# Kernel optimization log

Hardware: AMD Instinct MI355X
Metric: run time of the kernel (lower is better)

Reference implementation:

```python
import jax, jax.numpy as jnp
import numpy as np

N, L, D = 4096, 16, 768        # nodes, max name tokens, gpt2 embed dim
NH_NAME = 4                    # name-encoder attention heads
H, NH, NL, C = 1024, 8, 4, 16  # hidden, encoder heads, encoder layers, classes
XF = 256                       # raw node feature dim; feat_dim = XF + D = 1024
VOCAB = 50257


def _ln(x, g, b, eps=1e-5):
    m = jnp.mean(x, axis=-1, keepdims=True)
    v = jnp.var(x, axis=-1, keepdims=True)
    return (x - m) * jax.lax.rsqrt(v + eps) * g + b


def _mha(x, in_w, in_b, out_w, out_b, nh, key_mask=None):
    # x: [B, S, E]; in_w: [3E, E] (torch nn.MultiheadAttention packed qkv)
    B, S, E = x.shape
    dh = E // nh
    qkv = x @ in_w.T + in_b
    q, k, v = jnp.split(qkv, 3, axis=-1)
    q = q.reshape(B, S, nh, dh)
    k = k.reshape(B, S, nh, dh)
    v = v.reshape(B, S, nh, dh)
    scores = jnp.einsum('bqhd,bkhd->bhqk', q, k) / jnp.sqrt(jnp.asarray(dh, x.dtype))
    if key_mask is not None:
        scores = jnp.where(key_mask[:, None, None, :], scores, jnp.asarray(-1e9, x.dtype))
    a = jax.nn.softmax(scores, axis=-1)
    o = jnp.einsum('bhqk,bkhd->bqhd', a, v).reshape(B, S, E)
    return o @ out_w.T + out_b


def setup_inputs() -> dict:
    key = jax.random.key(0)
    ks = jax.random.split(key, 16)
    s = 0.02
    r = lambda i, shape: jax.random.normal(ks[i], shape, jnp.float32) * s
    return {
        'name_tokens': jax.random.randint(ks[0], (N, L), 0, VOCAB),
        'name_lens': jax.random.randint(ks[1], (N,), 1, L + 1),
        'x_feats': jax.random.normal(ks[2], (N, XF), jnp.float32),
        'wte': r(3, (VOCAB, D)),
        'mha_in_w': r(4, (3 * D, D)), 'mha_in_b': jnp.zeros((3 * D,), jnp.float32),
        'mha_out_w': r(5, (D, D)), 'mha_out_b': jnp.zeros((D,), jnp.float32),
        'bott_w': r(6, (H, XF + D)), 'bott_b': jnp.zeros((H,), jnp.float32),
        'enc_in_w': r(7, (NL, 3 * H, H)), 'enc_in_b': jnp.zeros((NL, 3 * H), jnp.float32),
        'enc_out_w': r(8, (NL, H, H)), 'enc_out_b': jnp.zeros((NL, H), jnp.float32),
        'enc_ln1_g': jnp.ones((NL, H), jnp.float32), 'enc_ln1_b': jnp.zeros((NL, H), jnp.float32),
        'enc_ln2_g': jnp.ones((NL, H), jnp.float32), 'enc_ln2_b': jnp.zeros((NL, H), jnp.float32),
        'enc_ff1_w': r(9, (NL, 2 * H, H)), 'enc_ff1_b': jnp.zeros((NL, 2 * H), jnp.float32),
        'enc_ff2_w': r(10, (NL, H, 2 * H)), 'enc_ff2_b': jnp.zeros((NL, H), jnp.float32),
        'cls_w': r(11, (C, H)), 'cls_b': jnp.zeros((C,), jnp.float32),
    }


def reference(name_tokens, name_lens, x_feats, wte,
              mha_in_w, mha_in_b, mha_out_w, mha_out_b,
              bott_w, bott_b,
              enc_in_w, enc_in_b, enc_out_w, enc_out_b,
              enc_ln1_g, enc_ln1_b, enc_ln2_g, enc_ln2_b,
              enc_ff1_w, enc_ff1_b, enc_ff2_w, enc_ff2_b,
              cls_w, cls_b):
    # --- GraphNameEncoder: batched over all N ragged name sequences ---
    mask = jnp.arange(L)[None, :] < name_lens[:, None]          # [N, L] valid-token mask
    emb = wte[name_tokens]                                      # [N, L, D]
    attn = _mha(emb, mha_in_w, mha_in_b, mha_out_w, mha_out_b, NH_NAME, key_mask=mask)
    name_emb = jnp.sum(jnp.where(mask[:, :, None], attn, 0.0), axis=1)  # [N, D]
    x = jnp.concatenate([x_feats, name_emb], axis=-1)           # [N, XF + D]
    # --- bottleneck ---
    x = x @ bott_w.T + bott_b                                   # [N, H]
    # --- TransformerEncoder on seq_len=1 (x.unsqueeze(1)), post-norm, relu ---
    h = x[:, None, :]                                           # [N, 1, H]
    for l in range(NL):
        a = _mha(h, enc_in_w[l], enc_in_b[l], enc_out_w[l], enc_out_b[l], NH)
        h = _ln(h + a, enc_ln1_g[l], enc_ln1_b[l])
        f = jax.nn.relu(h @ enc_ff1_w[l].T + enc_ff1_b[l]) @ enc_ff2_w[l].T + enc_ff2_b[l]
        h = _ln(h + f, enc_ln2_g[l], enc_ln2_b[l])
    out = h @ cls_w.T + cls_b                                   # [N, 1, C]
    return out[:, 0, :]                                         # squeeze -> [N, C]
```

## Files before the change

kernel.cpp:

```cpp
#include <hip/hip_runtime.h>

typedef unsigned short bf16_t;
typedef __attribute__((ext_vector_type(8))) __bf16 bf16x8;
typedef __attribute__((ext_vector_type(4))) float f32x4;

__device__ __forceinline__ float bf2f(unsigned v) { return __uint_as_float(v << 16); }
__device__ __forceinline__ bf16_t f2bf(float f) {
  unsigned u = __float_as_uint(f);
  return (bf16_t)((u + 0x7fffu + ((u >> 16) & 1u)) >> 16);
}
__device__ __forceinline__ unsigned pack2(float a, float b) {
  return (unsigned)f2bf(a) | ((unsigned)f2bf(b) << 16);
}

__device__ __forceinline__ void swz_decode(int& mt, int& nt) {
  const int NT = gridDim.x, MT = gridDim.y;
  int lin = blockIdx.y * NT + blockIdx.x;
  if ((MT & 7) == 0 && gridDim.z == 1) {
    int xcd = lin & 7;
    int j = lin >> 3;
    mt = (j / NT) * 8 + xcd;
    nt = j % NT;
  } else {
    mt = blockIdx.y;
    nt = blockIdx.x;
  }
}

__global__ __launch_bounds__(256) void scan_lens(const int* __restrict__ lens,
                                                 int* __restrict__ offs,
                                                 int* __restrict__ Mact) {
  __shared__ int wsum[4];
  const int t = threadIdx.x;
  int v[16]; int s = 0;
#pragma unroll
  for (int i = 0; i < 16; i++) { v[i] = lens[t * 16 + i]; s += v[i]; }
  const int lane = t & 63, w = t >> 6;
  int x = s;
#pragma unroll
  for (int o = 1; o < 64; o <<= 1) {
    int y = __shfl_up(x, o);
    if (lane >= o) x += y;
  }
  if (lane == 63) wsum[w] = x;
  __syncthreads();
  int base = 0;
  for (int i = 0; i < w; i++) base += wsum[i];
  int run = base + x - s;
#pragma unroll
  for (int i = 0; i < 16; i++) { offs[t * 16 + i] = run; run += v[i]; }
  if (t == 255) Mact[0] = run;
}

__global__ void cvt_f32_bf16(const float* __restrict__ src, bf16_t* __restrict__ dst, long n4) {
  long i = (long)blockIdx.x * blockDim.x + threadIdx.x;
  if (i >= n4) return;
  float4 v = ((const float4*)src)[i];
  ((uint2*)dst)[i] = make_uint2(pack2(v.x, v.y), pack2(v.z, v.w));
}

__global__ __launch_bounds__(256) void cvt_trans(const float* __restrict__ src,
                                                 bf16_t* __restrict__ dst) {
  __shared__ float tile[32][33];
  const int l = blockIdx.z;
  const int bx = blockIdx.x * 32;
  const int by = blockIdx.y * 32;
  const float* s = src + (size_t)l * 3 * 1024 * 1024 + 2 * 1024 * 1024;
  const int tx = threadIdx.x & 31, ty = threadIdx.x >> 5;
#pragma unroll
  for (int i = 0; i < 32; i += 8)
    tile[ty + i][tx] = s[(size_t)(by + ty + i) * 1024 + bx + tx];
  __syncthreads();
  bf16_t* d = dst + (size_t)l * 1024 * 1024;
#pragma unroll
  for (int i = 0; i < 32; i += 8)
    d[(size_t)(bx + ty + i) * 1024 + by + tx] = f2bf(tile[tx][ty + i]);
}

__global__ __launch_bounds__(256) void bias_comb(const float* __restrict__ enc_out_w,
                                                 const float* __restrict__ enc_in_b,
                                                 const float* __restrict__ enc_out_b,
                                                 float* __restrict__ bc) {
  const int l = blockIdx.y;
  const int wave = threadIdx.x >> 6, lane = threadIdx.x & 63;
  const float* w = enc_out_w + (size_t)l * 1024 * 1024;
  const float* bv = enc_in_b + (size_t)l * 3072 + 2048;
  for (int c = wave; c < 16; c += 4) {
    int i = blockIdx.x * 16 + c;
    const float* wr = w + (size_t)i * 1024;
    float acc = 0.f;
    for (int j = lane; j < 1024; j += 64) acc += wr[j] * bv[j];
#pragma unroll
    for (int o = 32; o > 0; o >>= 1) acc += __shfl_down(acc, o);
    if (lane == 0) bc[(size_t)l * 1024 + i] = acc + enc_out_b[(size_t)l * 1024 + i];
  }
}

__global__ void gather_emb_c(const int* __restrict__ tok, const int* __restrict__ lens,
                             const int* __restrict__ offs, const float* __restrict__ wte,
                             bf16_t* __restrict__ emb) {
  long i = (long)blockIdx.x * blockDim.x + threadIdx.x;
  if (i >= 65536L * 192L) return;
  long nl = i / 192; int cg = (int)(i % 192);
  int n = (int)(nl >> 4), l = (int)(nl & 15);
  if (l >= lens[n]) return;
  long ro = (long)offs[n] + l;
  int t = tok[nl];
  float4 v = *(const float4*)(wte + (long)t * 768 + cg * 4);
  ((uint2*)emb)[ro * 192 + cg] = make_uint2(pack2(v.x, v.y), pack2(v.z, v.w));
}

__global__ void xfeat_lenf(const float* __restrict__ xf, const int* __restrict__ lens,
                           bf16_t* __restrict__ x, float* __restrict__ lenf) {
  long i = (long)blockIdx.x * blockDim.x + threadIdx.x;
  if (i < 4096) lenf[i] = (float)lens[i];
  if (i >= 4096L * 64L) return;
  int row = (int)(i >> 6); int c4 = (int)(i & 63) * 4;
  float4 v = *(const float4*)(xf + (long)row * 256 + c4);
  *(uint2*)(x + (long)row * 1024 + c4) = make_uint2(pack2(v.x, v.y), pack2(v.z, v.w));
}

#define BM 128
#define BN 128
#define BK 32
#define SBT (BM * BK + BN * BK)

__device__ __forceinline__ void async16(const void* g, void* l) {
  __builtin_amdgcn_global_load_lds((const __attribute__((address_space(1))) void*)g,
                                   (__attribute__((address_space(3))) void*)l, 16, 0, 0);
}

__device__ __forceinline__ int swz4(int row) { return (row & 3) ^ ((row >> 2) & 3); }

__global__ __launch_bounds__(256, 4) void gemm_bt(
    const bf16_t* __restrict__ A, const bf16_t* __restrict__ W,
    const float* __restrict__ bias, bf16_t* __restrict__ C,
    int K, int ldc, const int* __restrict__ Mp,
    long sA, long sB, long sC) {
  int mt, nt;
  swz_decode(mt, nt);
  const int m0 = mt * BM;
  if (Mp != nullptr && m0 >= *Mp) return;
  __shared__ __attribute__((aligned(16))) bf16_t smem[2 * SBT];
  const int t = threadIdx.x;
  const int n0 = nt * BN;
  const int z = blockIdx.z;
  const int lane = t & 63;
  const int wr = t >> 7;
  const int wc = (t >> 6) & 1;
  const int quad = lane >> 4;
  const int r16 = lane & 15;

  f32x4 acc[4][4] = {};

  const int c0 = t, c1 = t + 256;
  const int row0 = c0 >> 2, kp0 = ((c0 & 3) ^ swz4(row0)) << 3;
  const int row1 = c1 >> 2, kp1 = ((c1 & 3) ^ swz4(row1)) << 3;
  const size_t oc0 = (size_t)(c0 & ~63) * 8;
  const size_t oc1 = (size_t)(c1 & ~63) * 8;
  const bf16_t* Ab = A + (size_t)z * sA + (size_t)m0 * K;
  const bf16_t* Wb = W + (size_t)z * sB + (size_t)n0 * K;
  bf16_t* Cb = C + (size_t)z * sC;

  auto stage = [&](int b, int k0) {
    bf16_t* As = smem + (size_t)b * SBT;
    bf16_t* Bs = As + BM * BK;
    async16(Ab + (size_t)row0 * K + k0 + kp0, As + oc0);
    async16(Ab + (size_t)row1 * K + k0 + kp1, As + oc1);
    async16(Wb + (size_t)row0 * K + k0 + kp0, Bs + oc0);
    async16(Wb + (size_t)row1 * K + k0 + kp1, Bs + oc1);
  };

  stage(0, 0);
  __syncthreads();
  int cur = 0;
  for (int k0 = 0; k0 < K; k0 += BK) {
    if (k0 + BK < K) stage(cur ^ 1, k0 + BK);
    const bf16_t* As = smem + (size_t)cur * SBT;
    const bf16_t* Bs = As + BM * BK;
    bf16x8 af[4], bfr[4];
#pragma unroll
    for (int i = 0; i < 4; i++) {
      int Ra = wr * 64 + i * 16 + r16;
      af[i]  = *(const bf16x8*)(As + Ra * BK + ((quad ^ swz4(Ra)) << 3));
      int Rb = wc * 64 + i * 16 + r16;
      bfr[i] = *(const bf16x8*)(Bs + Rb * BK + ((quad ^ swz4(Rb)) << 3));
    }
#pragma unroll
    for (int i = 0; i < 4; i++)
#pragma unroll
      for (int j = 0; j < 4; j++)
        acc[i][j] = __builtin_amdgcn_mfma_f32_16x16x32_bf16(af[i], bfr[j], acc[i][j], 0, 0, 0);
    __syncthreads();
    cur ^= 1;
  }

  const int ldcs = 136;
  bf16_t* Cs = smem;
#pragma unroll
  for (int s = 0; s < 4; s++) {
    if (wr == (s >> 1)) {
      const int ib = (s & 1) * 2;
#pragma unroll
      for (int i2 = 0; i2 < 2; i2++) {
        const int i = ib + i2;
#pragma unroll
        for (int j = 0; j < 4; j++) {
          int col = wc * 64 + j * 16 + r16;
          float bv = bias ? bias[n0 + col] : 0.0f;
#pragma unroll
          for (int r = 0; r < 4; r++)
            Cs[(i2 * 16 + quad * 4 + r) * ldcs + col] = f2bf(acc[i][j][r] + bv);
        }
      }
    }
    __syncthreads();
    {
      const int rl = t >> 4, cl = (t & 15) * 8;
#pragma unroll
      for (int p = 0; p < 2; p++) {
        int row = rl + p * 16;
        bf16x8 v = *(const bf16x8*)(Cs + row * ldcs + cl);
        *(bf16x8*)(Cb + (size_t)(m0 + s * 32 + row) * ldc + n0 + cl) = v;
      }
    }
    __syncthreads();
  }
}

#define S64 (128 * 32 + 64 * 32)

template <bool RELU>
__global__ __launch_bounds__(256, 6) void gemm128x64(
    const bf16_t* __restrict__ A, const bf16_t* __restrict__ W,
    const float* __restrict__ bias, const float* __restrict__ rowscale,
    bf16_t* __restrict__ C, int K, int ldc) {
  __shared__ __attribute__((aligned(16))) bf16_t smem[2 * S64];
  const int t = threadIdx.x;
  int mt, nt;
  swz_decode(mt, nt);
  const int m0 = mt * 128, n0 = nt * 64;
  const int lane = t & 63, w = t >> 6;
  const int quad = lane >> 4, r16 = lane & 15;
  f32x4 acc[2][4] = {};
  int rowA[2], kpA[2];
  size_t oA[2];
#pragma unroll
  for (int i = 0; i < 2; i++) {
    int c = t + i * 256;
    rowA[i] = c >> 2;
    kpA[i] = ((c & 3) ^ swz4(rowA[i])) << 3;
    oA[i] = (size_t)(c & ~63) * 8;
  }
  const int rowB = t >> 2;
  const int kpB = ((t & 3) ^ swz4(rowB)) << 3;
  const size_t oB = (size_t)(t & ~63) * 8;
  const bf16_t* Ab = A + (size_t)m0 * K;
  const bf16_t* Wb = W + (size_t)n0 * K;

  auto stage = [&](int b, int k0) {
    bf16_t* As = smem + (size_t)b * S64;
    bf16_t* Bs = As + 128 * 32;
    async16(Ab + (size_t)rowA[0] * K + k0 + kpA[0], As + oA[0]);
    async16(Ab + (size_t)rowA[1] * K + k0 + kpA[1], As + oA[1]);
    async16(Wb + (size_t)rowB * K + k0 + kpB, Bs + oB);
  };

  stage(0, 0);
  __syncthreads();
  int cur = 0;
  for (int k0 = 0; k0 < K; k0 += 32) {
    if (k0 + 32 < K) stage(cur ^ 1, k0 + 32);
    const bf16_t* As = smem + (size_t)cur * S64;
    const bf16_t* Bs = As + 128 * 32;
    bf16x8 af[2], bfr[4];
#pragma unroll
    for (int i = 0; i < 2; i++) {
      int Ra = w * 32 + i * 16 + r16;
      af[i] = *(const bf16x8*)(As + Ra * 32 + ((quad ^ swz4(Ra)) << 3));
    }
#pragma unroll
    for (int j = 0; j < 4; j++) {
      int Rb = j * 16 + r16;
      bfr[j] = *(const bf16x8*)(Bs + Rb * 32 + ((quad ^ swz4(Rb)) << 3));
    }
#pragma unroll
    for (int i = 0; i < 2; i++)
#pragma unroll
      for (int j = 0; j < 4; j++)
        acc[i][j] = __builtin_amdgcn_mfma_f32_16x16x32_bf16(af[i], bfr[j], acc[i][j], 0, 0, 0);
    __syncthreads();
    cur ^= 1;
  }

  const int ldcs = 72;
  bf16_t* Cs = smem;
#pragma unroll
  for (int i = 0; i < 2; i++) {
#pragma unroll
    for (int j = 0; j < 4; j++) {
      int col = j * 16 + r16;
      float bv = bias ? bias[n0 + col] : 0.0f;
#pragma unroll
      for (int r = 0; r < 4; r++) {
        int row = w * 32 + i * 16 + quad * 4 + r;
        float sc = rowscale ? rowscale[m0 + row] : 1.0f;
        float v = acc[i][j][r] + bv * sc;
        if (RELU) v = fmaxf(v, 0.0f);
        Cs[row * ldcs + col] = f2bf(v);
      }
    }
  }
  __syncthreads();
  {
    const int rl = t >> 3, cl = (t & 7) * 8;
#pragma unroll
    for (int p = 0; p < 4; p++) {
      int row = rl + p * 32;
      bf16x8 v = *(const bf16x8*)(Cs + row * ldcs + cl);
      *(bf16x8*)(C + (size_t)(m0 + row) * ldc + n0 + cl) = v;
    }
  }
}

__global__ __launch_bounds__(64) void attn_name(const bf16_t* __restrict__ qkv,
                                                const int* __restrict__ lens,
                                                const int* __restrict__ offs,
                                                bf16_t* __restrict__ s) {
  const int n = blockIdx.x, h = blockIdx.y;
  const int lane = threadIdx.x;
  __shared__ unsigned short qs[16][208];
  __shared__ unsigned short ks[16][208];
  __shared__ unsigned short vs[16][208];
  __shared__ float ps[16][16];
  __shared__ float wj[16];
  const int len = lens[n];
  const bf16_t* base = qkv + (size_t)offs[n] * 2304 + h * 192;
  for (int g = lane; g < len * 48; g += 64) {
    int row = g / 48, c4 = (g % 48) * 4;
    const bf16_t* p = base + (size_t)row * 2304 + c4;
    uint2 a;
    a = *(const uint2*)p;
    *(unsigned*)&qs[row][c4] = a.x; *(unsigned*)&qs[row][c4 + 2] = a.y;
    a = *(const uint2*)(p + 768);
    *(unsigned*)&ks[row][c4] = a.x; *(unsigned*)&ks[row][c4 + 2] = a.y;
    a = *(const uint2*)(p + 1536);
    *(unsigned*)&vs[row][c4] = a.x; *(unsigned*)&vs[row][c4 + 2] = a.y;
  }
  __syncthreads();
  {
    const int l = lane >> 2, j0 = (lane & 3) * 4;
    float s0 = 0, s1 = 0, s2 = 0, s3 = 0;
    for (int d = 0; d < 192; d++) {
      float q = bf2f(qs[l][d]);
      s0 += q * bf2f(ks[j0 + 0][d]);
      s1 += q * bf2f(ks[j0 + 1][d]);
      s2 += q * bf2f(ks[j0 + 2][d]);
      s3 += q * bf2f(ks[j0 + 3][d]);
    }
    const float sc = 0.07216878f;
    ps[l][j0 + 0] = s0 * sc; ps[l][j0 + 1] = s1 * sc;
    ps[l][j0 + 2] = s2 * sc; ps[l][j0 + 3] = s3 * sc;
  }
  __syncthreads();
  if (lane < 16) {
    float m = -1e30f;
    for (int j = 0; j < len; j++) m = fmaxf(m, ps[lane][j]);
    float sum = 0.f;
    for (int j = 0; j < len; j++) sum += __expf(ps[lane][j] - m);
    float inv = 1.0f / sum;
    for (int j = 0; j < 16; j++) ps[lane][j] = (j < len) ? __expf(ps[lane][j] - m) * inv : 0.0f;
  }
  __syncthreads();
  if (lane < 16) {
    float a = 0.f;
    for (int l2 = 0; l2 < len; l2++) a += ps[l2][lane];
    wj[lane] = a;
  }
  __syncthreads();
  for (int d = lane; d < 192; d += 64) {
    float a = 0.f;
    for (int j = 0; j < len; j++) a += wj[j] * bf2f(vs[j][d]);
    s[(size_t)n * 768 + h * 192 + d] = f2bf(a);
  }
}

__global__ __launch_bounds__(256) void ln_res(bf16_t* __restrict__ h, const bf16_t* __restrict__ d,
                                              const float* __restrict__ g, const float* __restrict__ b) {
  const int n = blockIdx.x, t = threadIdx.x;
  __shared__ float s1[4], s2[4];
  bf16_t* hr = h + (size_t)n * 1024;
  const bf16_t* dr = d + (size_t)n * 1024;
  float x[4];
  float sum = 0.f, ss = 0.f;
#pragma unroll
  for (int i = 0; i < 4; i++) {
    int c = t + i * 256;
    float v = bf2f(hr[c]) + bf2f(dr[c]);
    x[i] = v; sum += v; ss += v * v;
  }
#pragma unroll
  for (int o = 32; o > 0; o >>= 1) { sum += __shfl_down(sum, o); ss += __shfl_down(ss, o); }
  if ((t & 63) == 0) { s1[t >> 6] = sum; s2[t >> 6] = ss; }
  __syncthreads();
  sum = s1[0] + s1[1] + s1[2] + s1[3];
  ss  = s2[0] + s2[1] + s2[2] + s2[3];
  const float mean = sum * (1.0f / 1024.0f);
  const float var = ss * (1.0f / 1024.0f) - mean * mean;
  const float rstd = rsqrtf(var + 1e-5f);
#pragma unroll
  for (int i = 0; i < 4; i++) {
    int c = t + i * 256;
    hr[c] = f2bf((x[i] - mean) * rstd * g[c] + b[c]);
  }
}

__global__ __launch_bounds__(256) void cls_head(const bf16_t* __restrict__ h,
                                                const float* __restrict__ cw,
                                                const float* __restrict__ cb,
                                                float* __restrict__ out) {
  const int n = blockIdx.x, t = threadIdx.x, wave = t >> 6, lane = t & 63;
  const bf16_t* hr = h + (size_t)n * 1024;
  for (int c = wave; c < 16; c += 4) {
    const float* wr = cw + c * 1024;
    float acc = 0.f;
    for (int i = lane; i < 1024; i += 64) acc += bf2f(hr[i]) * wr[i];
#pragma unroll
    for (int o = 32; o > 0; o >>= 1) acc += __shfl_down(acc, o);
    if (lane == 0) out[(size_t)n * 16 + c] = acc + cb[c];
  }
}

extern "C" void kernel_launch(void* const* d_in, const int* in_sizes, int n_in,
                              void* d_out, int out_size, void* d_ws, size_t ws_size,
                              hipStream_t stream) {
  (void)in_sizes; (void)n_in; (void)out_size; (void)ws_size;
  const int* name_tokens = (const int*)d_in[0];
  const int* name_lens   = (const int*)d_in[1];
  const float* x_feats   = (const float*)d_in[2];
  const float* wte       = (const float*)d_in[3];
  const float* mha_in_w  = (const float*)d_in[4];
  const float* mha_in_b  = (const float*)d_in[5];
  const float* mha_out_w = (const float*)d_in[6];
  const float* mha_out_b = (const float*)d_in[7];
  const float* bott_w    = (const float*)d_in[8];
  const float* bott_b    = (const float*)d_in[9];
  const float* enc_in_w  = (const float*)d_in[10];
  const float* enc_in_b  = (const float*)d_in[11];
  const float* enc_out_w = (const float*)d_in[12];
  const float* enc_out_b = (const float*)d_in[13];
  const float* enc_ln1_g = (const float*)d_in[14];
  const float* enc_ln1_b = (const float*)d_in[15];
  const float* enc_ln2_g = (const float*)d_in[16];
  const float* enc_ln2_b = (const float*)d_in[17];
  const float* enc_ff1_w = (const float*)d_in[18];
  const float* enc_ff1_b = (const float*)d_in[19];
  const float* enc_ff2_w = (const float*)d_in[20];
  const float* enc_ff2_b = (const float*)d_in[21];
  const float* cls_w     = (const float*)d_in[22];
  const float* cls_b     = (const float*)d_in[23];
  float* out = (float*)d_out;

  char* base = (char*)d_ws;
  size_t off = 0;
  auto alloc = [&](size_t bytes) -> char* {
    char* p = base + off;
    off = (off + bytes + 255) & ~(size_t)255;
    return p;
  };
  bf16_t* w_qkv  = (bf16_t*)alloc((size_t)2304 * 768 * 2);
  bf16_t* w_out  = (bf16_t*)alloc((size_t)768 * 768 * 2);
  bf16_t* w_bott = (bf16_t*)alloc((size_t)1024 * 1024 * 2);
  bf16_t* w_vT   = (bf16_t*)alloc((size_t)4 * 1024 * 1024 * 2);
  bf16_t* w_enco = (bf16_t*)alloc((size_t)4 * 1024 * 1024 * 2);
  bf16_t* w_ff1  = (bf16_t*)alloc((size_t)4 * 2048 * 1024 * 2);
  bf16_t* w_ff2  = (bf16_t*)alloc((size_t)4 * 1024 * 2048 * 2);
  float*  lenf   = (float*)alloc((size_t)4096 * 4);
  int*    offs   = (int*)alloc((size_t)4096 * 4);
  int*    Mact   = (int*)alloc((size_t)256);
  char* reuse = alloc((size_t)65536 * 768 * 2);
  bf16_t* emb = (bf16_t*)reuse;
  bf16_t* s_  = (bf16_t*)reuse;
  bf16_t* x_  = (bf16_t*)(reuse + 6291456);
  bf16_t* h_  = (bf16_t*)(reuse + 6291456 + 8388608);
  bf16_t* v_  = (bf16_t*)(reuse + 6291456 + 2 * 8388608);
  bf16_t* a_  = (bf16_t*)(reuse + 6291456 + 3 * 8388608);
  bf16_t* f1_ = (bf16_t*)(reuse + 6291456 + 4 * 8388608);
  bf16_t* qkv = (bf16_t*)alloc((size_t)65536 * 2304 * 2);
  bf16_t* wc = (bf16_t*)qkv;
  float*  bc = (float*)((char*)qkv + (size_t)4 * 1024 * 1024 * 2);

  dim3 b256(256);
  auto g1 = [](long n4) { return dim3((unsigned)((n4 + 255) / 256)); };

  scan_lens<<<dim3(1), b256, 0, stream>>>(name_lens, offs, Mact);

  cvt_f32_bf16<<<g1(442368), b256, 0, stream>>>(mha_in_w, w_qkv, 442368L);
  cvt_f32_bf16<<<g1(147456), b256, 0, stream>>>(mha_out_w, w_out, 147456L);
  cvt_f32_bf16<<<g1(262144), b256, 0, stream>>>(bott_w, w_bott, 262144L);
  cvt_trans<<<dim3(32, 32, 4), b256, 0, stream>>>(enc_in_w, w_vT);
  cvt_f32_bf16<<<g1(1048576), b256, 0, stream>>>(enc_out_w, w_enco, 1048576L);
  cvt_f32_bf16<<<g1(2097152), b256, 0, stream>>>(enc_ff1_w, w_ff1, 2097152L);
  cvt_f32_bf16<<<g1(2097152), b256, 0, stream>>>(enc_ff2_w, w_ff2, 2097152L);

  gather_emb_c<<<dim3(49152), b256, 0, stream>>>(name_tokens, name_lens, offs, wte, emb);
  gemm_bt<<<dim3(18, 512), b256, 0, stream>>>(emb, w_qkv, mha_in_b, qkv, 768, 2304, Mact,
                                              0L, 0L, 0L);
  xfeat_lenf<<<dim3(1024), b256, 0, stream>>>(x_feats, name_lens, x_, lenf);
  attn_name<<<dim3(4096, 4), dim3(64), 0, stream>>>(qkv, name_lens, offs, s_);

  gemm_bt<<<dim3(8, 8, 4), b256, 0, stream>>>(
      w_enco, w_vT, (const float*)nullptr, wc, 1024, 1024, (const int*)nullptr,
      (long)1024 * 1024, (long)1024 * 1024, (long)1024 * 1024);
  bias_comb<<<dim3(64, 4), b256, 0, stream>>>(enc_out_w, enc_in_b, enc_out_b, bc);

  gemm128x64<false><<<dim3(12, 32), b256, 0, stream>>>(s_, w_out, mha_out_b, lenf,
                                                       x_ + 256, 768, 1024);
  gemm128x64<false><<<dim3(16, 32), b256, 0, stream>>>(x_, w_bott, bott_b,
                                                       (const float*)nullptr, h_, 1024, 1024);
  for (int l = 0; l < 4; l++) {
    gemm128x64<false><<<dim3(16, 32), b256, 0, stream>>>(
        h_, wc + (size_t)l * 1024 * 1024, bc + (size_t)l * 1024,
        (const float*)nullptr, a_, 1024, 1024);
    ln_res<<<dim3(4096), b256, 0, stream>>>(h_, a_, enc_ln1_g + l * 1024, enc_ln1_b + l * 1024);
    gemm128x64<true><<<dim3(32, 32), b256, 0, stream>>>(
        h_, w_ff1 + (size_t)l * 2048 * 1024, enc_ff1_b + l * 2048,
        (const float*)nullptr, f1_, 1024, 2048);
    gemm128x64<false><<<dim3(16, 32), b256, 0, stream>>>(
        f1_, w_ff2 + (size_t)l * 1024 * 2048, enc_ff2_b + l * 1024,
        (const float*)nullptr, v_, 2048, 1024);
    ln_res<<<dim3(4096), b256, 0, stream>>>(h_, v_, enc_ln2_g + l * 1024, enc_ln2_b + l * 1024);
  }
  cls_head<<<dim3(4096), b256, 0, stream>>>(h_, cls_w, cls_b, out);
}
```

Before: 1.229 ms.

## Use larger GEMM tiles: 256x128 for name QKV, 128x128 for encoder GEMMs

Adds a 256x128-tile GEMM kernel for the ragged name QKV projection. It is launched as three back-to-back grids covering the 256 possible M tiles, with early exit past the active row count. The encoder, bottleneck and name out-projection GEMMs move from 128x64 tiles to a 128x128 kernel that keeps the bias, row-scale and ReLU epilogue, raising arithmetic intensity per block and cutting global reloads. The costs are fewer blocks per GEMM on a many-CU GPU, lower occupancy from more registers, and extra launch overhead from splitting the QKV GEMM into three launches.

```diff
diff --git a/kernel.cpp b/kernel.cpp
--- a/kernel.cpp
+++ b/kernel.cpp
@@ -120,30 +120,234 @@
   *(uint2*)(x + (long)row * 1024 + c4) = make_uint2(pack2(v.x, v.y), pack2(v.z, v.w));
 }
 
+__device__ __forceinline__ void async16(const void* g, void* l) {
+  __builtin_amdgcn_global_load_lds((const __attribute__((address_space(1))) void*)g,
+                                   (__attribute__((address_space(3))) void*)l, 16, 0, 0);
+}
+
+__device__ __forceinline__ int swz4(int row) { return (row & 3) ^ ((row >> 2) & 3); }
+
+#define FBM 256
+#define FBN 128
+#define FBK 32
+#define FSB (FBM * FBK + FBN * FBK)
+
+__global__ __launch_bounds__(256, 2) void gemm_fat(
+    const bf16_t* __restrict__ A, const bf16_t* __restrict__ W,
+    const float* __restrict__ bias, bf16_t* __restrict__ C,
+    int K, int ldc, const int* __restrict__ Mp, int mbase) {
+  const int m0 = (mbase + blockIdx.y) * FBM;
+  if (Mp != nullptr && m0 >= *Mp) return;
+  __shared__ __attribute__((aligned(16))) bf16_t smem[2 * FSB];
+  const int t = threadIdx.x;
+  const int n0 = blockIdx.x * FBN;
+  const int lane = t & 63;
+  const int wr = t >> 7;
+  const int wc = (t >> 6) & 1;
+  const int quad = lane >> 4;
+  const int r16 = lane & 15;
+
+  f32x4 acc[8][4] = {};
+
+  int rowA[4], kpA[4]; size_t oA[4];
+#pragma unroll
+  for (int i = 0; i < 4; i++) {
+    int c = t + i * 256;
+    rowA[i] = c >> 2;
+    kpA[i] = ((c & 3) ^ swz4(rowA[i])) << 3;
+    oA[i] = (size_t)(c & ~63) * 8;
+  }
+  int rowB[2], kpB[2]; size_t oB[2];
+#pragma unroll
+  for (int i = 0; i < 2; i++) {
+    int c = t + i * 256;
+    rowB[i] = c >> 2;
+    kpB[i] = ((c & 3) ^ swz4(rowB[i])) << 3;
+    oB[i] = (size_t)(c & ~63) * 8;
+  }
+  const bf16_t* Ab = A + (size_t)m0 * K;
+  const bf16_t* Wb = W + (size_t)n0 * K;
+
+  auto stage = [&](int b, int k0) {
+    bf16_t* As = smem + (size_t)b * FSB;
+    bf16_t* Bs = As + FBM * FBK;
+#pragma unroll
+    for (int i = 0; i < 4; i++) async16(Ab + (size_t)rowA[i] * K + k0 + kpA[i], As + oA[i]);
+#pragma unroll
+    for (int i = 0; i < 2; i++) async16(Wb + (size_t)rowB[i] * K + k0 + kpB[i], Bs + oB[i]);
+  };
+
+  stage(0, 0);
+  __syncthreads();
+  int cur = 0;
+  for (int k0 = 0; k0 < K; k0 += FBK) {
+    if (k0 + FBK < K) stage(cur ^ 1, k0 + FBK);
+    const bf16_t* As = smem + (size_t)cur * FSB;
+    const bf16_t* Bs = As + FBM * FBK;
+    bf16x8 af[8], bfr[4];
+#pragma unroll
+    for (int i = 0; i < 8; i++) {
+      int Ra = wr * 128 + i * 16 + r16;
+      af[i] = *(const bf16x8*)(As + Ra * FBK + ((quad ^ swz4(Ra)) << 3));
+    }
+#pragma unroll
+    for (int j = 0; j < 4; j++) {
+      int Rb = wc * 64 + j * 16 + r16;
+      bfr[j] = *(const bf16x8*)(Bs + Rb * FBK + ((quad ^ swz4(Rb)) << 3));
+    }
+#pragma unroll
+    for (int i = 0; i < 8; i++)
+#pragma unroll
+      for (int j = 0; j < 4; j++)
+        acc[i][j] = __builtin_amdgcn_mfma_f32_16x16x32_bf16(af[i], bfr[j], acc[i][j], 0, 0, 0);
+    __syncthreads();
+    cur ^= 1;
+  }
+
+  const int ldcs = 136;
+  bf16_t* Cs = smem;
+#pragma unroll
+  for (int s = 0; s < 8; s++) {
+    if (wr == (s >> 2)) {
+      const int ib = (s & 3) * 2;
+#pragma unroll
+      for (int i2 = 0; i2 < 2; i2++) {
+        const int i = ib + i2;
+#pragma unroll
+        for (int j = 0; j < 4; j++) {
+          int col = wc * 64 + j * 16 + r16;
+          float bv = bias ? bias[n0 + col] : 0.0f;
+#pragma unroll
+          for (int r = 0; r < 4; r++)
+            Cs[(i2 * 16 + quad * 4 + r) * ldcs + col] = f2bf(acc[i][j][r] + bv);
+        }
+      }
+    }
+    __syncthreads();
+    {
+      const int rl = t >> 4, cl = (t & 15) * 8;
+#pragma unroll
+      for (int p = 0; p < 2; p++) {
+        int row = rl + p * 16;
+        bf16x8 v = *(const bf16x8*)(Cs + row * ldcs + cl);
+        *(bf16x8*)(C + (size_t)(m0 + s * 32 + row) * ldc + n0 + cl) = v;
+      }
+    }
+    __syncthreads();
+  }
+}
+
 #define BM 128
 #define BN 128
 #define BK 32
 #define SBT (BM * BK + BN * BK)
 
-__device__ __forceinline__ void async16(const void* g, void* l) {
-  __builtin_amdgcn_global_load_lds((const __attribute__((address_space(1))) void*)g,
-                                   (__attribute__((address_space(3))) void*)l, 16, 0, 0);
-}
-
-__device__ __forceinline__ int swz4(int row) { return (row & 3) ^ ((row >> 2) & 3); }
+template <bool RELU>
+__global__ __launch_bounds__(256, 4) void gemm128(
+    const bf16_t* __restrict__ A, const bf16_t* __restrict__ W,
+    const float* __restrict__ bias, const float* __restrict__ rowscale,
+    bf16_t* __restrict__ C, int K, int ldc) {
+  int mt, nt;
+  swz_decode(mt, nt);
+  const int m0 = mt * BM;
+  __shared__ __attribute__((aligned(16))) bf16_t smem[2 * SBT];
+  const int t = threadIdx.x;
+  const int n0 = nt * BN;
+  const int lane = t & 63;
+  const int wr = t >> 7;
+  const int wc = (t >> 6) & 1;
+  const int quad = lane >> 4;
+  const int r16 = lane & 15;
+
+  f32x4 acc[4][4] = {};
+
+  const int c0 = t, c1 = t + 256;
+  const int row0 = c0 >> 2, kp0 = ((c0 & 3) ^ swz4(row0)) << 3;
+  const int row1 = c1 >> 2, kp1 = ((c1 & 3) ^ swz4(row1)) << 3;
+  const size_t oc0 = (size_t)(c0 & ~63) * 8;
+  const size_t oc1 = (size_t)(c1 & ~63) * 8;
+  const bf16_t* Ab = A + (size_t)m0 * K;
+  const bf16_t* Wb = W + (size_t)n0 * K;
+
+  auto stage = [&](int b, int k0) {
+    bf16_t* As = smem + (size_t)b * SBT;
+    bf16_t* Bs = As + BM * BK;
+    async16(Ab + (size_t)row0 * K + k0 + kp0, As + oc0);
+    async16(Ab + (size_t)row1 * K + k0 + kp1, As + oc1);
+    async16(Wb + (size_t)row0 * K + k0 + kp0, Bs + oc0);
+    async16(Wb + (size_t)row1 * K + k0 + kp1, Bs + oc1);
+  };
+
+  stage(0, 0);
+  __syncthreads();
+  int cur = 0;
+  for (int k0 = 0; k0 < K; k0 += BK) {
+    if (k0 + BK < K) stage(cur ^ 1, k0 + BK);
+    const bf16_t* As = smem + (size_t)cur * SBT;
+    const bf16_t* Bs = As + BM * BK;
+    bf16x8 af[4], bfr[4];
+#pragma unroll
+    for (int i = 0; i < 4; i++) {
+      int Ra = wr * 64 + i * 16 + r16;
+      af[i]  = *(const bf16x8*)(As + Ra * BK + ((quad ^ swz4(Ra)) << 3));
+      int Rb = wc * 64 + i * 16 + r16;
+      bfr[i] = *(const bf16x8*)(Bs + Rb * BK + ((quad ^ swz4(Rb)) << 3));
+    }
+#pragma unroll
+    for (int i = 0; i < 4; i++)
+#pragma unroll
+      for (int j = 0; j < 4; j++)
+        acc[i][j] = __builtin_amdgcn_mfma_f32_16x16x32_bf16(af[i], bfr[j], acc[i][j], 0, 0, 0);
+    __syncthreads();
+    cur ^= 1;
+  }
+
+  const int ldcs = 136;
+  bf16_t* Cs = smem;
+#pragma unroll
+  for (int s = 0; s < 4; s++) {
+    if (wr == (s >> 1)) {
+      const int ib = (s & 1) * 2;
+#pragma unroll
+      for (int i2 = 0; i2 < 2; i2++) {
+        const int i = ib + i2;
+#pragma unroll
+        for (int j = 0; j < 4; j++) {
+          int col = wc * 64 + j * 16 + r16;
+          float bv = bias ? bias[n0 + col] : 0.0f;
+#pragma unroll
+          for (int r = 0; r < 4; r++) {
+            int grow = m0 + s * 32 + i2 * 16 + quad * 4 + r;
+            float sc = rowscale ? rowscale[grow] : 1.0f;
+            float v = acc[i][j][r] + bv * sc;
+            if (RELU) v = fmaxf(v, 0.0f);
+            Cs[(i2 * 16 + quad * 4 + r) * ldcs + col] = f2bf(v);
+          }
+        }
+      }
+    }
+    __syncthreads();
+    {
+      const int rl = t >> 4, cl = (t & 15) * 8;
+#pragma unroll
+      for (int p = 0; p < 2; p++) {
+        int row = rl + p * 16;
+        bf16x8 v = *(const bf16x8*)(Cs + row * ldcs + cl);
+        *(bf16x8*)(C + (size_t)(m0 + s * 32 + row) * ldc + n0 + cl) = v;
+      }
+    }
+    __syncthreads();
+  }
+}
 
 __global__ __launch_bounds__(256, 4) void gemm_bt(
     const bf16_t* __restrict__ A, const bf16_t* __restrict__ W,
     const float* __restrict__ bias, bf16_t* __restrict__ C,
-    int K, int ldc, const int* __restrict__ Mp,
-    long sA, long sB, long sC) {
-  int mt, nt;
-  swz_decode(mt, nt);
-  const int m0 = mt * BM;
-  if (Mp != nullptr && m0 >= *Mp) return;
+    int K, int ldc, long sA, long sB, long sC) {
+  const int m0 = blockIdx.y * BM;
   __shared__ __attribute__((aligned(16))) bf16_t smem[2 * SBT];
   const int t = threadIdx.x;
-  const int n0 = nt * BN;
+  const int n0 = blockIdx.x * BN;
   const int z = blockIdx.z;
   const int lane = t & 63;
   const int wr = t >> 7;
@@ -225,101 +429,6 @@
       }
     }
     __syncthreads();
-  }
-}
-
-#define S64 (128 * 32 + 64 * 32)
-
-template <bool RELU>
-__global__ __launch_bounds__(256, 6) void gemm128x64(
-    const bf16_t* __restrict__ A, const bf16_t* __restrict__ W,
-    const float* __restrict__ bias, const float* __restrict__ rowscale,
-    bf16_t* __restrict__ C, int K, int ldc) {
-  __shared__ __attribute__((aligned(16))) bf16_t smem[2 * S64];
-  const int t = threadIdx.x;
-  int mt, nt;
-  swz_decode(mt, nt);
-  const int m0 = mt * 128, n0 = nt * 64;
-  const int lane = t & 63, w = t >> 6;
-  const int quad = lane >> 4, r16 = lane & 15;
-  f32x4 acc[2][4] = {};
-  int rowA[2], kpA[2];
-  size_t oA[2];
-#pragma unroll
-  for (int i = 0; i < 2; i++) {
-    int c = t + i * 256;
-    rowA[i] = c >> 2;
-    kpA[i] = ((c & 3) ^ swz4(rowA[i])) << 3;
-    oA[i] = (size_t)(c & ~63) * 8;
-  }
-  const int rowB = t >> 2;
-  const int kpB = ((t & 3) ^ swz4(rowB)) << 3;
-  const size_t oB = (size_t)(t & ~63) * 8;
-  const bf16_t* Ab = A + (size_t)m0 * K;
-  const bf16_t* Wb = W + (size_t)n0 * K;
-
-  auto stage = [&](int b, int k0) {
-    bf16_t* As = smem + (size_t)b * S64;
-    bf16_t* Bs = As + 128 * 32;
-    async16(Ab + (size_t)rowA[0] * K + k0 + kpA[0], As + oA[0]);
-    async16(Ab + (size_t)rowA[1] * K + k0 + kpA[1], As + oA[1]);
-    async16(Wb + (size_t)rowB * K + k0 + kpB, Bs + oB);
-  };
-
-  stage(0, 0);
-  __syncthreads();
-  int cur = 0;
-  for (int k0 = 0; k0 < K; k0 += 32) {
-    if (k0 + 32 < K) stage(cur ^ 1, k0 + 32);
-    const bf16_t* As = smem + (size_t)cur * S64;
-    const bf16_t* Bs = As + 128 * 32;
-    bf16x8 af[2], bfr[4];
-#pragma unroll
-    for (int i = 0; i < 2; i++) {
-      int Ra = w * 32 + i * 16 + r16;
-      af[i] = *(const bf16x8*)(As + Ra * 32 + ((quad ^ swz4(Ra)) << 3));
-    }
-#pragma unroll
-    for (int j = 0; j < 4; j++) {
-      int Rb = j * 16 + r16;
-      bfr[j] = *(const bf16x8*)(Bs + Rb * 32 + ((quad ^ swz4(Rb)) << 3));
-    }
-#pragma unroll
-    for (int i = 0; i < 2; i++)
-#pragma unroll
-      for (int j = 0; j < 4; j++)
-        acc[i][j] = __builtin_amdgcn_mfma_f32_16x16x32_bf16(af[i], bfr[j], acc[i][j], 0, 0, 0);
-    __syncthreads();
-    cur ^= 1;
-  }
-
-  const int ldcs = 72;
-  bf16_t* Cs = smem;
-#pragma unroll
-  for (int i = 0; i < 2; i++) {
-#pragma unroll
-    for (int j = 0; j < 4; j++) {
-      int col = j * 16 + r16;
-      float bv = bias ? bias[n0 + col] : 0.0f;
-#pragma unroll
-      for (int r = 0; r < 4; r++) {
-        int row = w * 32 + i * 16 + quad * 4 + r;
-        float sc = rowscale ? rowscale[m0 + row] : 1.0f;
-        float v = acc[i][j][r] + bv * sc;
-        if (RELU) v = fmaxf(v, 0.0f);
-        Cs[row * ldcs + col] = f2bf(v);
-      }
-    }
-  }
-  __syncthreads();
-  {
-    const int rl = t >> 3, cl = (t & 7) * 8;
-#pragma unroll
-    for (int p = 0; p < 4; p++) {
-      int row = rl + p * 32;
-      bf16x8 v = *(const bf16x8*)(Cs + row * ldcs + cl);
-      *(bf16x8*)(C + (size_t)(m0 + row) * ldc + n0 + cl) = v;
-    }
   }
 }
 
@@ -504,29 +613,30 @@
   cvt_f32_bf16<<<g1(2097152), b256, 0, stream>>>(enc_ff2_w, w_ff2, 2097152L);
 
   gather_emb_c<<<dim3(49152), b256, 0, stream>>>(name_tokens, name_lens, offs, wte, emb);
-  gemm_bt<<<dim3(18, 512), b256, 0, stream>>>(emb, w_qkv, mha_in_b, qkv, 768, 2304, Mact,
-                                              0L, 0L, 0L);
+  gemm_fat<<<dim3(18, 86), b256, 0, stream>>>(emb, w_qkv, mha_in_b, qkv, 768, 2304, Mact, 0);
+  gemm_fat<<<dim3(18, 86), b256, 0, stream>>>(emb, w_qkv, mha_in_b, qkv, 768, 2304, Mact, 86);
+  gemm_fat<<<dim3(18, 84), b256, 0, stream>>>(emb, w_qkv, mha_in_b, qkv, 768, 2304, Mact, 172);
   xfeat_lenf<<<dim3(1024), b256, 0, stream>>>(x_feats, name_lens, x_, lenf);
   attn_name<<<dim3(4096, 4), dim3(64), 0, stream>>>(qkv, name_lens, offs, s_);
 
   gemm_bt<<<dim3(8, 8, 4), b256, 0, stream>>>(
-      w_enco, w_vT, (const float*)nullptr, wc, 1024, 1024, (const int*)nullptr,
+      w_enco, w_vT, (const float*)nullptr, wc, 1024, 1024,
       (long)1024 * 1024, (long)1024 * 1024, (long)1024 * 1024);
   bias_comb<<<dim3(64, 4), b256, 0, stream>>>(enc_out_w, enc_in_b, enc_out_b, bc);
 
-  gemm128x64<false><<<dim3(12, 32), b256, 0, stream>>>(s_, w_out, mha_out_b, lenf,
-                                                       x_ + 256, 768, 1024);
-  gemm128x64<false><<<dim3(16, 32), b256, 0, stream>>>(x_, w_bott, bott_b,
-                                                       (const float*)nullptr, h_, 1024, 1024);
+  gemm128<false><<<dim3(6, 32), b256, 0, stream>>>(s_, w_out, mha_out_b, lenf,
+                                                   x_ + 256, 768, 1024);
+  gemm128<false><<<dim3(8, 32), b256, 0, stream>>>(x_, w_bott, bott_b,
+                                                   (const float*)nullptr, h_, 1024, 1024);
   for (int l = 0; l < 4; l++) {
-    gemm128x64<false><<<dim3(16, 32), b256, 0, stream>>>(
+    gemm128<false><<<dim3(8, 32), b256, 0, stream>>>(
         h_, wc + (size_t)l * 1024 * 1024, bc + (size_t)l * 1024,
         (const float*)nullptr, a_, 1024, 1024);
     ln_res<<<dim3(4096), b256, 0, stream>>>(h_, a_, enc_ln1_g + l * 1024, enc_ln1_b + l * 1024);
-    gemm128x64<true><<<dim3(32, 32), b256, 0, stream>>>(
+    gemm128<true><<<dim3(16, 32), b256, 0, stream>>>(
         h_, w_ff1 + (size_t)l * 2048 * 1024, enc_ff1_b + l * 2048,
         (const float*)nullptr, f1_, 1024, 2048);
-    gemm128x64<false><<<dim3(16, 32), b256, 0, stream>>>(
+    gemm128<false><<<dim3(8, 32), b256, 0, stream>>>(
         f1_, w_ff2 + (size_t)l * 1024 * 2048, enc_ff2_b + l * 1024,
         (const float*)nullptr, v_, 2048, 1024);
     ln_res<<<dim3(4096), b256, 0, stream>>>(h_, v_, enc_ln2_g + l * 1024, enc_ln2_b + l * 1024);
```

Result: slower. 1.325 ms (+7.9%).
